# Kernel tuning notes

Hardware: AMD Instinct MI355X
Metric: run time of the kernel (lower is better)

The kernel has to match this reference:

```python
import jax, jax.numpy as jnp
import numpy as np

D = 64            # number of devices (leaves hold D/8 each)
B = 65536         # batch of states
FEAT = 5 + 4 * D  # 261
HID = 128


def setup_inputs() -> dict:
    key = jax.random.key(0)
    ks = jax.random.split(key, 10)
    def nrm(k, shape, s=0.1):
        return jax.random.normal(k, shape, jnp.float32) * s
    return {
        "x": jax.random.normal(ks[0], (B, FEAT), jnp.float32),
        # gate params per depth d: 2^d nodes, weight dim 5 + 4*D/2^d
        "w0": nrm(ks[1], (1, 5 + 4 * D)),
        "b0": jnp.zeros((1,), jnp.float32),
        "w1": nrm(ks[2], (2, 5 + 4 * (D // 2))),
        "b1": jnp.zeros((2,), jnp.float32),
        "w2": nrm(ks[3], (4, 5 + 4 * (D // 4))),
        "b2": jnp.zeros((4,), jnp.float32),
        # leaf prob_dist (torch inits to zeros; random here for a non-trivial baseline)
        "leaf_probs": nrm(ks[4], (8, D // 8), 1.0),
        # critic MLP
        "Wc1": nrm(ks[5], (FEAT, HID)),
        "bc1": jnp.zeros((HID,), jnp.float32),
        "Wc2": nrm(ks[6], (HID, 1)),
        "bc2": jnp.zeros((1,), jnp.float32),
    }


def reference(x, w0, b0, w1, b1, w2, b2, leaf_probs, Wc1, bc1, Wc2, bc2):
    # Batched deterministic ClusterTree routing (exploration disabled).
    x5 = x[:, :5]                       # (B, 5) global features
    dev = x[:, 5:].reshape(B, D, 4)     # (B, D, 4) per-device features
    node = jnp.zeros((B,), jnp.int32)   # current node index at each depth
    cum = jnp.ones((B,), x.dtype)       # product of gate values along path
    for d, (wd, bd) in enumerate([(w0, b0), (w1, b1), (w2, b2)]):
        nd = D >> d                     # devices per node at this depth
        off = node * nd                 # contiguous-cluster start offset
        idx = off[:, None] + jnp.arange(nd)                     # (B, nd)
        dslice = jnp.take_along_axis(dev, idx[:, :, None], 1)   # (B, nd, 4)
        w = wd[node]                    # (B, 5 + 4*nd)
        gate = (jnp.sum(x5 * w[:, :5], -1)
                + jnp.sum(dslice.reshape(B, -1) * w[:, 5:], -1)
                + bd[node])
        val = jax.nn.sigmoid(gate)
        cum = cum * val                 # torch: val * child_output, recursively
        node = node * 2 + (val >= 0.5).astype(jnp.int32)
    p = cum[:, None] * leaf_probs[node]                 # (B, D//8)
    v = jax.nn.relu(x @ Wc1 + bc1) @ Wc2 + bc2          # (B, 1) critic
    return p, v
```

## Files before the change

### kernel.cpp

```cpp
#include <hip/hip_runtime.h>
#include <hip/hip_bf16.h>
#include <stdint.h>

#define NB    65536
#define FEATN 261
#define HIDN  128
#define NSTEP 17
#define SROW  296

#define ROWSF 64
#define NTHRF 512

typedef __attribute__((ext_vector_type(8)))  short bf16x8;
typedef __attribute__((ext_vector_type(16))) float f32x16;
typedef float f32x4u __attribute__((ext_vector_type(4), aligned(4)));

#define MFMA32(A, B, C) __builtin_amdgcn_mfma_f32_32x32x16_bf16(A, B, C, 0, 0, 0)

__device__ __forceinline__ uint16_t f2b(float v) {
    __hip_bfloat16 b = __float2bfloat16(v);
    return *reinterpret_cast<uint16_t*>(&b);
}

__device__ __forceinline__ float sigmoidf(float g) {
    return 1.f / (1.f + __expf(-g));
}

#define RED16(v) do { v += __shfl_xor(v, 1); v += __shfl_xor(v, 2); \
                      v += __shfl_xor(v, 4); v += __shfl_xor(v, 8); } while (0)

__global__ void prep_kernel(const float* __restrict__ Wc1,
                            uint16_t* __restrict__ wsB)
{
    int t = blockIdx.x * 256 + threadIdx.x;
    if (t < NSTEP * 4 * 64) {
        int p = t >> 6, l = t & 63;
        int s = p >> 2, nt = p & 3;
        int n = nt * 32 + (l & 31);
        int kb = 16 * s + 8 * (l >> 5);
        uint16_t hw[8];
        #pragma unroll
        for (int j = 0; j < 8; ++j) {
            int k = kb + j;
            float v = (k < FEATN) ? Wc1[(size_t)k * HIDN + n] : 0.f;
            hw[j] = f2b(v);
        }
        *reinterpret_cast<uint4*>(wsB + (size_t)p * 512 + l * 8) =
            *reinterpret_cast<uint4*>(hw);
    }
}

__global__ __launch_bounds__(NTHRF, 4) void fused_kernel(
    const float* __restrict__ x,
    const float* __restrict__ w0, const float* __restrict__ b0,
    const float* __restrict__ w1, const float* __restrict__ b1,
    const float* __restrict__ w2, const float* __restrict__ b2,
    const float* __restrict__ leaf,
    const uint16_t* __restrict__ wsB,
    const float* __restrict__ bc1, const float* __restrict__ Wc2,
    const float* __restrict__ bc2,
    float* __restrict__ out_p, float* __restrict__ out_v)
{
    __shared__ uint16_t Axs[ROWSF * SROW];
    __shared__ float bc1s[HIDN];
    __shared__ float wc2s[HIDN];
    __shared__ float vpart[ROWSF * 4];

    const int tid = threadIdx.x;
    const int rowBase = blockIdx.x * ROWSF;

    if (tid < HIDN) { bc1s[tid] = bc1[tid]; wc2s[tid] = Wc2[tid]; }
    if (tid < ROWSF) {
        uint16_t* rp = Axs + tid * SROW;
        rp[261] = 0;
        *reinterpret_cast<uint32_t*>(rp + 262) = 0u;
        uint4 z; z.x = z.y = z.z = z.w = 0u;
        *reinterpret_cast<uint4*>(rp + 264) = z;
        *reinterpret_cast<uint4*>(rp + 272) = z;
        *reinterpret_cast<uint4*>(rp + 280) = z;
        *reinterpret_cast<uint4*>(rp + 288) = z;
    }

    const int s = tid & 15;
    const int g = tid >> 4;

    f32x4u w0q[4];
    #pragma unroll
    for (int j = 0; j < 4; ++j)
        w0q[j] = *reinterpret_cast<const f32x4u*>(w0 + 64 * j + 4 * s);
    const float w0t = (s < 5) ? w0[256 + s] : 0.f;

    float w1v[4][4], w2v[4][4];
    #pragma unroll
    for (int j = 0; j < 4; ++j)
        #pragma unroll
        for (int c = 0; c < 4; ++c) {
            int e = 64 * j + 4 * s + c;
            w1v[j][c] = w1[(e < 133) ? e : e + 5];
            int n2 = (e < 5) ? 0 : ((e - 5) >> 6);
            w2v[j][c] = w2[e + 5 * n2];
        }
    const float w1t = (s < 5) ? w1[261 + s] : 0.f;
    const float w2t = (s < 5) ? w2[271 + s] : 0.f;

    const float xw1b  = (s < 5) ? w1[133 + s] : 0.f;
    const float xw2_1 = (s < 5) ? w2[ 69 + s] : 0.f;
    const float xw2_2 = (s < 5) ? w2[138 + s] : 0.f;
    const float xw2_3 = (s < 5) ? w2[207 + s] : 0.f;

    const float b0s  = b0[0];
    const float b1s0 = b1[0], b1s1 = b1[1];
    const float b2s0 = b2[0], b2s1 = b2[1], b2s2 = b2[2], b2s3 = b2[3];

    f32x4u xq[2][4];
    float xt[2], xs5[2];
    #pragma unroll
    for (int r2 = 0; r2 < 2; ++r2) {
        const float* xr = x + (size_t)(rowBase + r2 * 32 + g) * FEATN;
        #pragma unroll
        for (int j = 0; j < 4; ++j)
            xq[r2][j] = *reinterpret_cast<const f32x4u*>(xr + 64 * j + 4 * s);
        xt[r2]  = (s < 5) ? xr[256 + s] : 0.f;
        xs5[r2] = (s < 5) ? xr[s]       : 0.f;
    }

    #pragma unroll
    for (int r2 = 0; r2 < 2; ++r2) {
        uint16_t* rp = Axs + (r2 * 32 + g) * SROW;
        #pragma unroll
        for (int j = 0; j < 4; ++j) {
            uint32_t p0w = (uint32_t)f2b(xq[r2][j][0]) | ((uint32_t)f2b(xq[r2][j][1]) << 16);
            uint32_t p1w = (uint32_t)f2b(xq[r2][j][2]) | ((uint32_t)f2b(xq[r2][j][3]) << 16);
            uint2 pk; pk.x = p0w; pk.y = p1w;
            *reinterpret_cast<uint2*>(rp + 64 * j + 4 * s) = pk;
        }
        if (s < 5) rp[256 + s] = f2b(xt[r2]);
    }

    #pragma unroll
    for (int r2 = 0; r2 < 2; ++r2) {
        const int row = rowBase + r2 * 32 + g;

        float p0 = 0.f, p1a = 0.f, p1b = 0.f;
        float p2_0 = 0.f, p2_1 = 0.f, p2_2 = 0.f, p2_3 = 0.f;
        #pragma unroll
        for (int j = 0; j < 4; ++j)
            #pragma unroll
            for (int c = 0; c < 4; ++c) {
                const float xv = xq[r2][j][c];
                const bool lo = (4 * s + c) < 5;
                p0 += xv * w0q[j][c];
                const float t1 = xv * w1v[j][c];
                const float t2 = xv * w2v[j][c];
                if (j == 0) {
                    p1a += t1;
                    p2_0 += t2;
                } else if (j == 1) {
                    p1a += t1;
                    p2_0 += lo ? t2 : 0.f;  p2_1 += lo ? 0.f : t2;
                } else if (j == 2) {
                    p1a += lo ? t1 : 0.f;   p1b += lo ? 0.f : t1;
                    p2_1 += lo ? t2 : 0.f;  p2_2 += lo ? 0.f : t2;
                } else {
                    p1b += t1;
                    p2_2 += lo ? t2 : 0.f;  p2_3 += lo ? 0.f : t2;
                }
            }
        p0   += xt[r2] * w0t;
        p1b  += xt[r2] * w1t;
        p2_3 += xt[r2] * w2t;
        p1b  += xs5[r2] * xw1b;
        p2_1 += xs5[r2] * xw2_1;
        p2_2 += xs5[r2] * xw2_2;
        p2_3 += xs5[r2] * xw2_3;

        RED16(p0);
        const float gate0 = p0 + b0s;
        int nn = (gate0 >= 0.f) ? 1 : 0;
        float cum = sigmoidf(gate0);

        float p1 = nn ? p1b : p1a;
        RED16(p1);
        const float gate1 = p1 + (nn ? b1s1 : b1s0);
        nn = nn * 2 + ((gate1 >= 0.f) ? 1 : 0);
        cum *= sigmoidf(gate1);

        float p2 = (nn & 2) ? ((nn & 1) ? p2_3 : p2_2)
                            : ((nn & 1) ? p2_1 : p2_0);
        RED16(p2);
        const float gate2 = p2 + ((nn & 2) ? ((nn & 1) ? b2s3 : b2s2)
                                           : ((nn & 1) ? b2s1 : b2s0));
        nn = nn * 2 + ((gate2 >= 0.f) ? 1 : 0);
        cum *= sigmoidf(gate2);

        if (s < 8)
            out_p[(size_t)row * 8 + s] = cum * leaf[nn * 8 + s];
    }

    __syncthreads();

    const int lane = tid & 63;
    const int w    = tid >> 6;
    const int mt   = w >> 2;
    const int nt   = w & 3;

    const uint16_t* arow = Axs + (mt * 32 + (lane & 31)) * SROW + (lane >> 5) * 8;
    const uint16_t* bgl  = wsB + (size_t)nt * 512 + lane * 8;

    f32x16 acc = {};
    #pragma unroll
    for (int ss = 0; ss < NSTEP; ++ss) {
        bf16x8 af = *reinterpret_cast<const bf16x8*>(arow + ss * 16);
        bf16x8 bf = *reinterpret_cast<const bf16x8*>(bgl + (size_t)(ss * 4) * 512);
        acc = MFMA32(af, bf, acc);
    }

    {
        const int c = lane & 31;
        const int q = lane >> 5;
        const int n = nt * 32 + c;
        const float bb = bc1s[n], ww = wc2s[n];

        float pv[16];
        #pragma unroll
        for (int reg = 0; reg < 16; ++reg) {
            float h = acc[reg] + bb; h = h > 0.f ? h : 0.f;
            float t = h * ww;
            t += __shfl_xor(t, 1);
            t += __shfl_xor(t, 2);
            t += __shfl_xor(t, 4);
            t += __shfl_xor(t, 8);
            t += __shfl_xor(t, 16);
            pv[reg] = t;
        }
        #pragma unroll
        for (int reg = 0; reg < 16; ++reg) {
            if (c == reg) {
                int row_local = (reg & 3) + 8 * (reg >> 2) + 4 * q;
                vpart[(mt * 32 + row_local) * 4 + nt] = pv[reg];
            }
        }
    }
    __syncthreads();
    if (tid < ROWSF)
        out_v[rowBase + tid] = (vpart[tid * 4] + vpart[tid * 4 + 1])
                             + (vpart[tid * 4 + 2] + vpart[tid * 4 + 3]) + bc2[0];
}

extern "C" void kernel_launch(void* const* d_in, const int* in_sizes, int n_in,
                              void* d_out, int out_size, void* d_ws, size_t ws_size,
                              hipStream_t stream) {
    const float* x    = (const float*)d_in[0];
    const float* w0   = (const float*)d_in[1];
    const float* b0   = (const float*)d_in[2];
    const float* w1   = (const float*)d_in[3];
    const float* b1   = (const float*)d_in[4];
    const float* w2   = (const float*)d_in[5];
    const float* b2   = (const float*)d_in[6];
    const float* leaf = (const float*)d_in[7];
    const float* Wc1  = (const float*)d_in[8];
    const float* bc1  = (const float*)d_in[9];
    const float* Wc2  = (const float*)d_in[10];
    const float* bc2  = (const float*)d_in[11];

    uint16_t* wsB = (uint16_t*)d_ws;

    float* out_p = (float*)d_out;
    float* out_v = out_p + (size_t)NB * 8;

    prep_kernel<<<17, 256, 0, stream>>>(Wc1, wsB);
    fused_kernel<<<NB / ROWSF, NTHRF, 0, stream>>>(
        x, w0, b0, w1, b1, w2, b2, leaf, wsB, bc1, Wc2, bc2, out_p, out_v);
}
```

Baseline: 134.5 us.

## Stage x tile into LDS via direct global-to-LDS loads with smaller blocks

Loads each block's x rows into LDS as fp32 with global_load_lds dword transfers, which are contiguous and coalesced, instead of each thread doing unaligned strided 16-byte global loads per row. The fp32 LDS buffer is then reused in place for the bf16 MFMA A-tile after a barrier. Blocks shrink from 64 rows/512 threads to 32 rows/256 threads, so each wave owns one 32-column N tile. The cost is extra barriers and an explicit vmcnt wait; the larger per-row LDS footprint may also limit occupancy.

```diff
diff --git a/kernel.cpp b/kernel.cpp
--- a/kernel.cpp
+++ b/kernel.cpp
@@ -7,13 +7,14 @@
 #define HIDN  128
 #define NSTEP 17
 #define SROW  296
-
-#define ROWSF 64
-#define NTHRF 512
+#define FPAD  272
+
+#define ROWSF 32
+#define NTHRF 256
 
 typedef __attribute__((ext_vector_type(8)))  short bf16x8;
 typedef __attribute__((ext_vector_type(16))) float f32x16;
-typedef float f32x4u __attribute__((ext_vector_type(4), aligned(4)));
+typedef float f32x4a __attribute__((ext_vector_type(4)));
 
 #define MFMA32(A, B, C) __builtin_amdgcn_mfma_f32_32x32x16_bf16(A, B, C, 0, 0, 0)
 
@@ -24,6 +25,12 @@
 
 __device__ __forceinline__ float sigmoidf(float g) {
     return 1.f / (1.f + __expf(-g));
+}
+
+__device__ __forceinline__ void gl_lds4(const void* g, void* l) {
+    __builtin_amdgcn_global_load_lds(
+        (const __attribute__((address_space(1))) void*)g,
+        (__attribute__((address_space(3))) void*)l, 4, 0, 0);
 }
 
 #define RED16(v) do { v += __shfl_xor(v, 1); v += __shfl_xor(v, 2); \
@@ -61,33 +68,43 @@
     const float* __restrict__ bc2,
     float* __restrict__ out_p, float* __restrict__ out_v)
 {
-    __shared__ uint16_t Axs[ROWSF * SROW];
-    __shared__ float bc1s[HIDN];
-    __shared__ float wc2s[HIDN];
-    __shared__ float vpart[ROWSF * 4];
-
-    const int tid = threadIdx.x;
+    __shared__ __align__(16) unsigned char lds_raw[ROWSF * FPAD * 4 + 1536];
+    float*    Xf    = (float*)lds_raw;
+    uint16_t* Axs   = (uint16_t*)lds_raw;
+    float*    bc1s  = (float*)(lds_raw + ROWSF * FPAD * 4);
+    float*    wc2s  = bc1s + HIDN;
+    float*    vpart = wc2s + HIDN;
+
+    const int tid  = threadIdx.x;
+    const int lane = tid & 63;
+    const int w    = tid >> 6;
     const int rowBase = blockIdx.x * ROWSF;
 
+    {
+        const float* xbase = x + (size_t)rowBase * FEATN;
+        #pragma unroll
+        for (int k = 0; k < 34; ++k) {
+            const int c = k * 4 + w;
+            int p   = c * 64 + lane;
+            int r   = (int)((unsigned)p / FPAD);
+            int col = p - r * FPAD;
+            col = (col < FEATN) ? col : (FEATN - 1);
+            gl_lds4(xbase + (size_t)r * FEATN + col,
+                    (char*)Xf + (size_t)c * 256);
+        }
+    }
+
     if (tid < HIDN) { bc1s[tid] = bc1[tid]; wc2s[tid] = Wc2[tid]; }
-    if (tid < ROWSF) {
-        uint16_t* rp = Axs + tid * SROW;
-        rp[261] = 0;
-        *reinterpret_cast<uint32_t*>(rp + 262) = 0u;
-        uint4 z; z.x = z.y = z.z = z.w = 0u;
-        *reinterpret_cast<uint4*>(rp + 264) = z;
-        *reinterpret_cast<uint4*>(rp + 272) = z;
-        *reinterpret_cast<uint4*>(rp + 280) = z;
-        *reinterpret_cast<uint4*>(rp + 288) = z;
-    }
 
     const int s = tid & 15;
     const int g = tid >> 4;
 
-    f32x4u w0q[4];
-    #pragma unroll
-    for (int j = 0; j < 4; ++j)
-        w0q[j] = *reinterpret_cast<const f32x4u*>(w0 + 64 * j + 4 * s);
+    f32x4a w0q[4];
+    #pragma unroll
+    for (int j = 0; j < 4; ++j) {
+        const float* p4 = w0 + 64 * j + 4 * s;
+        w0q[j] = f32x4a{p4[0], p4[1], p4[2], p4[3]};
+    }
     const float w0t = (s < 5) ? w0[256 + s] : 0.f;
 
     float w1v[4][4], w2v[4][4];
@@ -112,21 +129,29 @@
     const float b1s0 = b1[0], b1s1 = b1[1];
     const float b2s0 = b2[0], b2s1 = b2[1], b2s2 = b2[2], b2s3 = b2[3];
 
-    f32x4u xq[2][4];
-    float xt[2], xs5[2];
+    asm volatile("s_waitcnt vmcnt(0)" ::: "memory");
+    __syncthreads();
+
+    f32x4a xq[2][4];
+    float xt[2], x5v[2];
     #pragma unroll
     for (int r2 = 0; r2 < 2; ++r2) {
-        const float* xr = x + (size_t)(rowBase + r2 * 32 + g) * FEATN;
+        const float* fr = Xf + (size_t)(r2 * 16 + g) * FPAD;
         #pragma unroll
         for (int j = 0; j < 4; ++j)
-            xq[r2][j] = *reinterpret_cast<const f32x4u*>(xr + 64 * j + 4 * s);
-        xt[r2]  = (s < 5) ? xr[256 + s] : 0.f;
-        xs5[r2] = (s < 5) ? xr[s]       : 0.f;
-    }
+            xq[r2][j] = *(const f32x4a*)(fr + 64 * j + 4 * s);
+        xt[r2]  = (s < 5) ? fr[256 + s] : 0.f;
+        x5v[r2] = (s < 5) ? fr[s]       : 0.f;
+    }
+
+    __syncthreads();
 
     #pragma unroll
     for (int r2 = 0; r2 < 2; ++r2) {
-        uint16_t* rp = Axs + (r2 * 32 + g) * SROW;
+        const int rl  = r2 * 16 + g;
+        const int row = rowBase + rl;
+        uint16_t* rp = Axs + (size_t)rl * SROW;
+
         #pragma unroll
         for (int j = 0; j < 4; ++j) {
             uint32_t p0w = (uint32_t)f2b(xq[r2][j][0]) | ((uint32_t)f2b(xq[r2][j][1]) << 16);
@@ -134,12 +159,15 @@
             uint2 pk; pk.x = p0w; pk.y = p1w;
             *reinterpret_cast<uint2*>(rp + 64 * j + 4 * s) = pk;
         }
-        if (s < 5) rp[256 + s] = f2b(xt[r2]);
-    }
-
-    #pragma unroll
-    for (int r2 = 0; r2 < 2; ++r2) {
-        const int row = rowBase + r2 * 32 + g;
+        if (s < 4) rp[256 + s] = f2b(xt[r2]);
+        if (s == 4) {
+            uint2 pk; pk.x = (uint32_t)f2b(xt[r2]); pk.y = 0u;
+            *reinterpret_cast<uint2*>(rp + 260) = pk;
+        }
+        if (s < 8) {
+            uint2 z; z.x = 0u; z.y = 0u;
+            *reinterpret_cast<uint2*>(rp + 264 + 4 * s) = z;
+        }
 
         float p0 = 0.f, p1a = 0.f, p1b = 0.f;
         float p2_0 = 0.f, p2_1 = 0.f, p2_2 = 0.f, p2_3 = 0.f;
@@ -169,10 +197,10 @@
         p0   += xt[r2] * w0t;
         p1b  += xt[r2] * w1t;
         p2_3 += xt[r2] * w2t;
-        p1b  += xs5[r2] * xw1b;
-        p2_1 += xs5[r2] * xw2_1;
-        p2_2 += xs5[r2] * xw2_2;
-        p2_3 += xs5[r2] * xw2_3;
+        p1b  += x5v[r2] * xw1b;
+        p2_1 += x5v[r2] * xw2_1;
+        p2_2 += x5v[r2] * xw2_2;
+        p2_3 += x5v[r2] * xw2_3;
 
         RED16(p0);
         const float gate0 = p0 + b0s;
@@ -199,13 +227,8 @@
 
     __syncthreads();
 
-    const int lane = tid & 63;
-    const int w    = tid >> 6;
-    const int mt   = w >> 2;
-    const int nt   = w & 3;
-
-    const uint16_t* arow = Axs + (mt * 32 + (lane & 31)) * SROW + (lane >> 5) * 8;
-    const uint16_t* bgl  = wsB + (size_t)nt * 512 + lane * 8;
+    const uint16_t* arow = Axs + (size_t)(lane & 31) * SROW + (lane >> 5) * 8;
+    const uint16_t* bgl  = wsB + (size_t)w * 512 + lane * 8;
 
     f32x16 acc = {};
     #pragma unroll
@@ -218,7 +241,7 @@
     {
         const int c = lane & 31;
         const int q = lane >> 5;
-        const int n = nt * 32 + c;
+        const int n = w * 32 + c;
         const float bb = bc1s[n], ww = wc2s[n];
 
         float pv[16];
@@ -237,7 +260,7 @@
         for (int reg = 0; reg < 16; ++reg) {
             if (c == reg) {
                 int row_local = (reg & 3) + 8 * (reg >> 2) + 4 * q;
-                vpart[(mt * 32 + row_local) * 4 + nt] = pv[reg];
+                vpart[row_local * 4 + w] = pv[reg];
             }
         }
     }
```

Measured after the change: 135.7 us. About the same (+0.9%).
